# Kernel optimization log

Hardware: AMD Instinct MI355X
Metric: run time of the kernel (lower is better)

## Reference

```python
import jax, jax.numpy as jnp
import numpy as np

D_MODEL = 2048
NUM_HEADS = 16
D_K = D_MODEL // NUM_HEADS
MAX_SEQ_LEN = 2048


def setup_inputs() -> dict:
    key = jax.random.key(0)
    ks = jax.random.split(key, 9)
    s = 1.0 / np.sqrt(D_MODEL)
    x = jax.random.normal(ks[0], (4, 2048, D_MODEL), dtype=jnp.float32)
    Wq = jax.random.normal(ks[1], (D_MODEL, D_MODEL), dtype=jnp.float32) * s
    bq = jnp.zeros((D_MODEL,), dtype=jnp.float32)
    Wk = jax.random.normal(ks[2], (D_MODEL, D_MODEL), dtype=jnp.float32) * s
    bk = jnp.zeros((D_MODEL,), dtype=jnp.float32)
    Wv = jax.random.normal(ks[3], (D_MODEL, D_MODEL), dtype=jnp.float32) * s
    bv = jnp.zeros((D_MODEL,), dtype=jnp.float32)
    Wo = jax.random.normal(ks[4], (D_MODEL, D_MODEL), dtype=jnp.float32) * s
    bo = jnp.zeros((D_MODEL,), dtype=jnp.float32)
    return {"x": x, "Wq": Wq, "bq": bq, "Wk": Wk, "bk": bk,
            "Wv": Wv, "bv": bv, "Wo": Wo, "bo": bo}


def _rope_tables(seq_len, d_k, dtype):
    # GPT-NeoX style rotate-half RoPE tables: [seq_len, d_k]
    inv_freq = 1.0 / (10000.0 ** (np.arange(0, d_k, 2, dtype=np.float32) / d_k))
    pos = np.arange(seq_len, dtype=np.float32)
    freqs = np.outer(pos, inv_freq)              # [S, d_k/2]
    emb = np.concatenate([freqs, freqs], axis=-1)  # [S, d_k]
    return jnp.asarray(np.cos(emb), dtype=dtype), jnp.asarray(np.sin(emb), dtype=dtype)


def _apply_rope(x, cos, sin):
    # x: [B, H, S, d_k]; rotate-half
    x1, x2 = jnp.split(x, 2, axis=-1)
    rotated = jnp.concatenate([-x2, x1], axis=-1)
    return x * cos + rotated * sin


def reference(x, Wq, bq, Wk, bk, Wv, bv, Wo, bo):
    B, S, _ = x.shape
    cos, sin = _rope_tables(S, D_K, x.dtype)  # [S, d_k]

    def split_heads(t):  # [B,S,D] -> [B,H,S,d_k]
        return t.reshape(B, S, NUM_HEADS, D_K).transpose(0, 2, 1, 3)

    q = split_heads(x @ Wq.T + bq)
    k = split_heads(x @ Wk.T + bk)
    v = split_heads(x @ Wv.T + bv)

    q = _apply_rope(q, cos, sin)
    k = _apply_rope(k, cos, sin)

    scale = 1.0 / jnp.sqrt(jnp.asarray(D_K, dtype=x.dtype))
    scores = jnp.einsum("bhqd,bhkd->bhqk", q, k) * scale
    attn = jax.nn.softmax(scores, axis=-1)
    out = jnp.einsum("bhqk,bhkd->bhqd", attn, v)  # [B,H,S,d_k]
    out = out.transpose(0, 2, 1, 3).reshape(B, S, D_MODEL)
    return out @ Wo.T + bo
```

## Files before the change

kernel.cpp:

```cpp
#include <hip/hip_runtime.h>
#include <hip/hip_bf16.h>
#include <math.h>

typedef __bf16 bf16;
typedef __bf16 bf16x2 __attribute__((ext_vector_type(2)));
typedef __bf16 bf16x4 __attribute__((ext_vector_type(4)));
typedef __bf16 bf16x8 __attribute__((ext_vector_type(8)));
typedef float f32x4 __attribute__((ext_vector_type(4)));

#define D_MODEL 2048
#define SEQ 2048
#define BATCH 4
#define NH 16
#define DK 128

typedef const __attribute__((address_space(1))) void* as1_ptr;
typedef __attribute__((address_space(3))) void* as3_ptr;

__device__ __forceinline__ void gld_lds16(const bf16* g, bf16* l) {
  __builtin_amdgcn_global_load_lds((as1_ptr)g, (as3_ptr)l, 16, 0, 0);
}

__global__ void cvt_kernel(const float* __restrict__ in, bf16* __restrict__ out, int n8) {
  int i = blockIdx.x * 256 + threadIdx.x;
  if (i >= n8) return;
  long base = (long)i * 8;
  const float4* p = (const float4*)(in + base);
  float4 a = p[0], b = p[1];
  bf16x8 v;
  v[0] = (bf16)a.x; v[1] = (bf16)a.y; v[2] = (bf16)a.z; v[3] = (bf16)a.w;
  v[4] = (bf16)b.x; v[5] = (bf16)b.y; v[6] = (bf16)b.z; v[7] = (bf16)b.w;
  *(bf16x8*)(out + base) = v;
}

__global__ void cvt4_kernel(const float* a, const float* b, const float* c, const float* d,
                            bf16* oa, bf16* ob, bf16* oc, bf16* od) {
  const float* in; bf16* out;
  switch (blockIdx.y) {
    case 0: in = a; out = oa; break;
    case 1: in = b; out = ob; break;
    case 2: in = c; out = oc; break;
    default: in = d; out = od; break;
  }
  int i = blockIdx.x * 256 + threadIdx.x;
  long base = (long)i * 8;
  const float4* p = (const float4*)(in + base);
  float4 x = p[0], y = p[1];
  bf16x8 v;
  v[0] = (bf16)x.x; v[1] = (bf16)x.y; v[2] = (bf16)x.z; v[3] = (bf16)x.w;
  v[4] = (bf16)y.x; v[5] = (bf16)y.y; v[6] = (bf16)y.z; v[7] = (bf16)y.w;
  *(bf16x8*)(out + base) = v;
}

template<int OUT_F32, int BIAS_ROW>
__global__ __launch_bounds__(256, 2)
void gemm_nt(const bf16* __restrict__ A, const bf16* __restrict__ B,
             const float* __restrict__ bias, void* __restrict__ Cout, int K, int ldc)
{
  __shared__ alignas(16) bf16 As[128 * 32];
  __shared__ alignas(16) bf16 Bs[128 * 32];
  const int tid  = threadIdx.x;
  const int wave = tid >> 6, lane = tid & 63;
  const int quad = lane >> 4, l16 = lane & 15;
  const int n0 = blockIdx.x * 128, m0 = blockIdx.y * 128;
  const int wm = (wave >> 1) * 64, wn = (wave & 1) * 64;

  const int srow = tid >> 2, scol = (tid & 3) * 8;
  const bf16* Ag1 = A + (long)(m0 + srow) * K + scol;
  const bf16* Ag2 = Ag1 + (long)64 * K;
  const bf16* Bg1 = B + (long)(n0 + srow) * K + scol;
  const bf16* Bg2 = Bg1 + (long)64 * K;
  bf16* Asw = As + wave * 512;
  bf16* Bsw = Bs + wave * 512;

  f32x4 acc[4][4] = {};
  for (int k0 = 0; k0 < K; k0 += 32) {
    __syncthreads();
    gld_lds16(Ag1 + k0, Asw);
    gld_lds16(Ag2 + k0, Asw + 2048);
    gld_lds16(Bg1 + k0, Bsw);
    gld_lds16(Bg2 + k0, Bsw + 2048);
    __syncthreads();
    bf16x8 Af[4], Bf[4];
    for (int mi = 0; mi < 4; mi++)
      Af[mi] = *(const bf16x8*)(&As[(wm + mi * 16 + l16) * 32 + quad * 8]);
    for (int ni = 0; ni < 4; ni++)
      Bf[ni] = *(const bf16x8*)(&Bs[(wn + ni * 16 + l16) * 32 + quad * 8]);
    for (int mi = 0; mi < 4; mi++)
      for (int ni = 0; ni < 4; ni++)
        acc[mi][ni] = __builtin_amdgcn_mfma_f32_16x16x32_bf16(Af[mi], Bf[ni], acc[mi][ni], 0, 0, 0);
  }

  float bv[4];
  if (!BIAS_ROW)
    for (int ni = 0; ni < 4; ni++) bv[ni] = bias[n0 + wn + ni * 16 + l16];
  for (int mi = 0; mi < 4; mi++)
    for (int r = 0; r < 4; r++) {
      long row = m0 + wm + mi * 16 + quad * 4 + r;
      float bm = BIAS_ROW ? bias[row] : 0.0f;
      for (int ni = 0; ni < 4; ni++) {
        float v = acc[mi][ni][r] + (BIAS_ROW ? bm : bv[ni]);
        long idx = row * (long)ldc + n0 + wn + ni * 16 + l16;
        if (OUT_F32) ((float*)Cout)[idx] = v;
        else         ((bf16*)Cout)[idx] = (bf16)v;
      }
    }
}

__global__ void ropetab_kernel(float* __restrict__ ctab) {
  int idx = blockIdx.x * 256 + threadIdx.x;
  int j = idx & 63, p = idx >> 6;
  float f = exp2f(-(float)j * 0.20762050593046f);
  float th = (float)p * f;
  ctab[idx * 2]     = cosf(th);
  ctab[idx * 2 + 1] = sinf(th);
}

__global__ void rope_kernel(bf16* __restrict__ Q, bf16* __restrict__ K,
                            const float* __restrict__ ctab) {
  long idx = (long)blockIdx.x * 256 + threadIdx.x;
  bf16* P = blockIdx.y ? K : Q;
  int i2 = (int)(idx & 31);
  int h  = (int)((idx >> 5) & 15);
  long row = idx >> 9;
  int pos = (int)(row & (SEQ - 1));
  float4 cs = *(const float4*)(ctab + ((long)pos * 64 + 2 * i2) * 2);
  long base = row * D_MODEL + h * DK + 2 * i2;
  bf16x2 x1 = *(bf16x2*)(P + base);
  bf16x2 x2 = *(bf16x2*)(P + base + 64);
  bf16x2 y1, y2;
  y1[0] = (bf16)((float)x1[0] * cs.x - (float)x2[0] * cs.y);
  y2[0] = (bf16)((float)x2[0] * cs.x + (float)x1[0] * cs.y);
  y1[1] = (bf16)((float)x1[1] * cs.z - (float)x2[1] * cs.w);
  y2[1] = (bf16)((float)x2[1] * cs.z + (float)x1[1] * cs.w);
  *(bf16x2*)(P + base)      = y1;
  *(bf16x2*)(P + base + 64) = y2;
}

__global__ __launch_bounds__(256, 2)
void attn_kernel(const bf16* __restrict__ Q, const bf16* __restrict__ K,
                 const bf16* __restrict__ Vt, bf16* __restrict__ O)
{
  __shared__ alignas(16) bf16 Ks[64 * 128];
  __shared__ alignas(16) bf16 Vts[128 * 64];
  __shared__ alignas(16) bf16 Ps[128 * 72];
  const int tid  = threadIdx.x;
  const int wave = tid >> 6, lane = tid & 63;
  const int quad = lane >> 4, l16 = lane & 15;
  const int qt = blockIdx.x, bh = blockIdx.y;
  const int b = bh >> 4, h = bh & 15;
  const long qrow0 = (long)b * SEQ + qt * 128;
  const bf16* Qb = Q + qrow0 * D_MODEL + h * DK;
  const bf16* Kb = K + (long)b * SEQ * D_MODEL + h * DK;
  const bf16* Vb = Vt + (long)(h * DK) * (BATCH * SEQ) + b * SEQ;

  bf16x8 Qf[2][4];
  for (int ni = 0; ni < 2; ni++)
    for (int ks = 0; ks < 4; ks++)
      Qf[ni][ks] = *(const bf16x8*)(Qb + (long)(wave * 32 + ni * 16 + l16) * D_MODEL + ks * 32 + quad * 8);

  const bf16* Ksrc[4]; const bf16* Vsrc[4];
  for (int i = 0; i < 4; i++) {
    int g = wave * 4 + i;
    int rk = 4 * g + (lane >> 4);
    int ck = l16 ^ (rk & 7);
    Ksrc[i] = Kb + (long)rk * D_MODEL + ck * 8;
    int rv = 8 * g + (lane >> 3);
    int cv = (lane & 7) ^ (rv & 7);
    Vsrc[i] = Vb + (long)rv * (BATCH * SEQ) + cv * 8;
  }

  f32x4 Oacc[8][2] = {};
  float lsum[2] = {0.0f, 0.0f};
  const float kSc = 0.088388347648318447f * 1.4426950408889634f;
  const int swz = l16 & 7;

  for (int kt = 0; kt < SEQ; kt += 64) {
    __syncthreads();
    for (int i = 0; i < 4; i++)
      gld_lds16(Ksrc[i] + (long)kt * D_MODEL, Ks + (wave * 4 + i) * 512);
    for (int i = 0; i < 4; i++)
      gld_lds16(Vsrc[i] + kt, Vts + (wave * 4 + i) * 512);
    __syncthreads();

    f32x4 Sc[4][2] = {};
    for (int ks = 0; ks < 4; ks++) {
      bf16x8 Kf[4];
      for (int si = 0; si < 4; si++) {
        int c = (ks * 4 + quad) ^ swz;
        Kf[si] = *(const bf16x8*)(&Ks[(si * 16 + l16) * 128 + c * 8]);
      }
      for (int si = 0; si < 4; si++)
        for (int ni = 0; ni < 2; ni++)
          Sc[si][ni] = __builtin_amdgcn_mfma_f32_16x16x32_bf16(Kf[si], Qf[ni][ks], Sc[si][ni], 0, 0, 0);
    }

    for (int si = 0; si < 4; si++)
      for (int ni = 0; ni < 2; ni++) {
        bf16x4 pk;
        for (int r = 0; r < 4; r++) {
          float p = exp2f(Sc[si][ni][r] * kSc);
          lsum[ni] += p;
          pk[r] = (bf16)p;
        }
        *(bf16x4*)(&Ps[(wave * 32 + ni * 16 + l16) * 72 + si * 16 + quad * 4]) = pk;
      }

    for (int k2 = 0; k2 < 2; k2++) {
      bf16x8 Pf[2];
      for (int ni = 0; ni < 2; ni++)
        Pf[ni] = *(const bf16x8*)(&Ps[(wave * 32 + ni * 16 + l16) * 72 + k2 * 32 + quad * 8]);
      for (int mi = 0; mi < 8; mi++) {
        int c = (k2 * 4 + quad) ^ swz;
        bf16x8 Vf = *(const bf16x8*)(&Vts[(mi * 16 + l16) * 64 + c * 8]);
        for (int ni = 0; ni < 2; ni++)
          Oacc[mi][ni] = __builtin_amdgcn_mfma_f32_16x16x32_bf16(Vf, Pf[ni], Oacc[mi][ni], 0, 0, 0);
      }
    }
  }

  for (int ni = 0; ni < 2; ni++) {
    lsum[ni] += __shfl_xor(lsum[ni], 16);
    lsum[ni] += __shfl_xor(lsum[ni], 32);
  }

  for (int ni = 0; ni < 2; ni++) {
    float rinv = 1.0f / lsum[ni];
    long rowbase = (qrow0 + wave * 32 + ni * 16 + l16) * (long)D_MODEL + h * DK + quad * 4;
    for (int mi = 0; mi < 8; mi++) {
      bf16x4 o;
      for (int r = 0; r < 4; r++) o[r] = (bf16)(Oacc[mi][ni][r] * rinv);
      *(bf16x4*)(O + rowbase + mi * 16) = o;
    }
  }
}

extern "C" void kernel_launch(void* const* d_in, const int* in_sizes, int n_in,
                              void* d_out, int out_size, void* d_ws, size_t ws_size,
                              hipStream_t stream) {
  const float* x  = (const float*)d_in[0];
  const float* Wq = (const float*)d_in[1];
  const float* bq = (const float*)d_in[2];
  const float* Wk = (const float*)d_in[3];
  const float* bk = (const float*)d_in[4];
  const float* Wv = (const float*)d_in[5];
  const float* bv = (const float*)d_in[6];
  const float* Wo = (const float*)d_in[7];
  const float* bo = (const float*)d_in[8];
  float* out = (float*)d_out;

  bf16* ws = (bf16*)d_ws;
  bf16* xb  = ws;
  bf16* Wqb = ws + 16777216;
  bf16* Wkb = ws + 20971520;
  bf16* Wvb = ws + 25165824;
  bf16* Wob = ws + 29360128;
  bf16* Qp  = ws + 33554432;
  bf16* Kp  = ws + 50331648;
  bf16* VtF = ws + 67108864;
  float* ctab = (float*)ws;
  bf16* O   = xb;

  cvt_kernel<<<8192, 256, 0, stream>>>(x, xb, 2097152);
  cvt4_kernel<<<dim3(2048, 4), 256, 0, stream>>>(Wq, Wk, Wv, Wo, Wqb, Wkb, Wvb, Wob);

  dim3 gg(16, 64);
  gemm_nt<0, 0><<<gg, 256, 0, stream>>>(xb, Wqb, bq, Qp, 2048, 2048);
  gemm_nt<0, 0><<<gg, 256, 0, stream>>>(xb, Wkb, bk, Kp, 2048, 2048);
  gemm_nt<0, 1><<<dim3(64, 16), 256, 0, stream>>>(Wvb, xb, bv, VtF, 2048, 8192);

  ropetab_kernel<<<512, 256, 0, stream>>>(ctab);
  rope_kernel<<<dim3(16384, 2), 256, 0, stream>>>(Qp, Kp, ctab);

  attn_kernel<<<dim3(16, 64), 256, 0, stream>>>(Qp, Kp, VtF, O);

  gemm_nt<1, 0><<<gg, 256, 0, stream>>>(O, Wob, bo, out, 2048, 2048);
}
```

Before: 698.7 us.

## Double-buffer K/V tiles in attention and split score tile into halves

Adds ping-pong LDS buffers for the K and V tiles so the async global-to-LDS load of the next tile overlaps compute on the current one, cutting one barrier per iteration. Each 64-key tile is processed in two 32-key halves, which halves the P scratch buffer and shrinks the live score registers. MFMA sections are bracketed with s_setprio to favour matrix issue. The extra buffers raise LDS use, which may limit the two-blocks-per-CU occupancy target. Each half writes Ps and then reads it back with no barrier in between; this is presumably safe because each wave only touches its own Ps rows.

```diff
diff --git a/kernel.cpp b/kernel.cpp
--- a/kernel.cpp
+++ b/kernel.cpp
@@ -141,9 +141,9 @@
 void attn_kernel(const bf16* __restrict__ Q, const bf16* __restrict__ K,
                  const bf16* __restrict__ Vt, bf16* __restrict__ O)
 {
-  __shared__ alignas(16) bf16 Ks[64 * 128];
-  __shared__ alignas(16) bf16 Vts[128 * 64];
-  __shared__ alignas(16) bf16 Ps[128 * 72];
+  __shared__ alignas(16) bf16 Ks[2][64 * 128];
+  __shared__ alignas(16) bf16 Vts[2][128 * 64];
+  __shared__ alignas(16) bf16 Ps[128 * 36];
   const int tid  = threadIdx.x;
   const int wave = tid >> 6, lane = tid & 63;
   const int quad = lane >> 4, l16 = lane & 15;
@@ -175,48 +175,63 @@
   const float kSc = 0.088388347648318447f * 1.4426950408889634f;
   const int swz = l16 & 7;
 
-  for (int kt = 0; kt < SEQ; kt += 64) {
-    __syncthreads();
-    for (int i = 0; i < 4; i++)
-      gld_lds16(Ksrc[i] + (long)kt * D_MODEL, Ks + (wave * 4 + i) * 512);
-    for (int i = 0; i < 4; i++)
-      gld_lds16(Vsrc[i] + kt, Vts + (wave * 4 + i) * 512);
-    __syncthreads();
-
-    f32x4 Sc[4][2] = {};
-    for (int ks = 0; ks < 4; ks++) {
-      bf16x8 Kf[4];
-      for (int si = 0; si < 4; si++) {
-        int c = (ks * 4 + quad) ^ swz;
-        Kf[si] = *(const bf16x8*)(&Ks[(si * 16 + l16) * 128 + c * 8]);
+  for (int i = 0; i < 4; i++) gld_lds16(Ksrc[i], &Ks[0][(wave * 4 + i) * 512]);
+  for (int i = 0; i < 4; i++) gld_lds16(Vsrc[i], &Vts[0][(wave * 4 + i) * 512]);
+  __syncthreads();
+
+  int cur = 0;
+  for (int kt = 64; kt <= SEQ; kt += 64) {
+    if (kt < SEQ) {
+      for (int i = 0; i < 4; i++)
+        gld_lds16(Ksrc[i] + (long)kt * D_MODEL, &Ks[cur ^ 1][(wave * 4 + i) * 512]);
+      for (int i = 0; i < 4; i++)
+        gld_lds16(Vsrc[i] + kt, &Vts[cur ^ 1][(wave * 4 + i) * 512]);
+    }
+    const bf16* Ksb = Ks[cur];
+    const bf16* Vsb = Vts[cur];
+
+    for (int hh = 0; hh < 2; hh++) {
+      f32x4 Sc[2][2] = {};
+      __builtin_amdgcn_s_setprio(1);
+      for (int ks = 0; ks < 4; ks++) {
+        bf16x8 Kf[2];
+        for (int j = 0; j < 2; j++) {
+          int si = hh * 2 + j;
+          int c = (ks * 4 + quad) ^ swz;
+          Kf[j] = *(const bf16x8*)(&Ksb[(si * 16 + l16) * 128 + c * 8]);
+        }
+        for (int j = 0; j < 2; j++)
+          for (int ni = 0; ni < 2; ni++)
+            Sc[j][ni] = __builtin_amdgcn_mfma_f32_16x16x32_bf16(Kf[j], Qf[ni][ks], Sc[j][ni], 0, 0, 0);
       }
-      for (int si = 0; si < 4; si++)
-        for (int ni = 0; ni < 2; ni++)
-          Sc[si][ni] = __builtin_amdgcn_mfma_f32_16x16x32_bf16(Kf[si], Qf[ni][ks], Sc[si][ni], 0, 0, 0);
-    }
-
-    for (int si = 0; si < 4; si++)
-      for (int ni = 0; ni < 2; ni++) {
-        bf16x4 pk;
-        for (int r = 0; r < 4; r++) {
-          float p = exp2f(Sc[si][ni][r] * kSc);
-          lsum[ni] += p;
-          pk[r] = (bf16)p;
+      __builtin_amdgcn_s_setprio(0);
+
+      for (int j = 0; j < 2; j++)
+        for (int ni = 0; ni < 2; ni++) {
+          bf16x4 pk;
+          for (int r = 0; r < 4; r++) {
+            float p = exp2f(Sc[j][ni][r] * kSc);
+            lsum[ni] += p;
+            pk[r] = (bf16)p;
+          }
+          *(bf16x4*)(&Ps[(wave * 32 + ni * 16 + l16) * 36 + j * 16 + quad * 4]) = pk;
         }
-        *(bf16x4*)(&Ps[(wave * 32 + ni * 16 + l16) * 72 + si * 16 + quad * 4]) = pk;
-      }
-
-    for (int k2 = 0; k2 < 2; k2++) {
+
+      __builtin_amdgcn_s_setprio(1);
       bf16x8 Pf[2];
       for (int ni = 0; ni < 2; ni++)
-        Pf[ni] = *(const bf16x8*)(&Ps[(wave * 32 + ni * 16 + l16) * 72 + k2 * 32 + quad * 8]);
+        Pf[ni] = *(const bf16x8*)(&Ps[(wave * 32 + ni * 16 + l16) * 36 + quad * 8]);
       for (int mi = 0; mi < 8; mi++) {
-        int c = (k2 * 4 + quad) ^ swz;
-        bf16x8 Vf = *(const bf16x8*)(&Vts[(mi * 16 + l16) * 64 + c * 8]);
+        int c = (hh * 4 + quad) ^ swz;
+        bf16x8 Vf = *(const bf16x8*)(&Vsb[(mi * 16 + l16) * 64 + c * 8]);
         for (int ni = 0; ni < 2; ni++)
           Oacc[mi][ni] = __builtin_amdgcn_mfma_f32_16x16x32_bf16(Vf, Pf[ni], Oacc[mi][ni], 0, 0, 0);
       }
-    }
+      __builtin_amdgcn_s_setprio(0);
+    }
+
+    __syncthreads();
+    cur ^= 1;
   }
 
   for (int ni = 0; ni < 2; ni++) {
```

Measured after the change: 697.4 us. About the same (-0.2%).
